# Kernel tuning notes

Measured on AMD Instinct MI355X. Metric: run time of the kernel, lower is better.

The kernel has to match this reference:

```python
import jax, jax.numpy as jnp
import numpy as np

B, S, D, P, H = 32, 1024, 512, 720, 4   # batch, seq_len (=codebook_size), enc_in, pred_len, heads
COMMIT_W, ORTHO_W = 1.0, 0.8


def setup_inputs() -> dict:
    key = jax.random.key(0)
    ks = jax.random.split(key, 6)
    return {
        "x": jax.random.normal(ks[0], (B, S, D), jnp.float32),
        "w_in": jax.random.normal(ks[1], (H * D, D), jnp.float32) * 0.02,   # project_in: dim -> heads*dim
        "b_in": jnp.zeros((H * D,), jnp.float32),
        "embed": jax.random.normal(ks[2], (H, S, D), jnp.float32),          # per-head codebook [h, C, d]
        "w_out": jax.random.normal(ks[3], (D, H * D), jnp.float32) * 0.02,  # project_out: heads*dim -> dim
        "b_out": jnp.zeros((D,), jnp.float32),
        "w_lin": jax.random.normal(ks[4], (P, S), jnp.float32) * 0.02,      # Linear over time axis
        "b_lin": jnp.zeros((P,), jnp.float32),
    }


def reference(x, w_in, b_in, embed, w_out, b_out, w_lin, b_lin):
    C = embed.shape[1]
    # Normalization: subtract last timestep (detached)
    seq_last = jax.lax.stop_gradient(x[:, -1:, :])          # [B,1,D]
    x0 = x - seq_last                                       # [B,S,D]

    # --- VectorQuantize ---
    xi = x0 @ w_in.T + b_in                                 # [B,S,H*D] project_in
    # 'b n (h d) -> h (b n) d' (separate codebook per head)
    f = xi.reshape(B, S, H, D).transpose(2, 0, 1, 3).reshape(H, B * S, D)
    # squared-euclidean distances to codes: [H, B*S, C]
    d2 = (jnp.sum(f * f, -1, keepdims=True)
          - 2.0 * jnp.einsum('hnd,hcd->hnc', f, embed)
          + jnp.sum(embed * embed, -1)[:, None, :])
    ind = jnp.argmin(d2, axis=-1)                           # [H, B*S]
    q = jnp.take_along_axis(embed, ind[:, :, None], axis=1)  # gather -> [H, B*S, D]

    # commitment loss (learnable codebook => quantize NOT detached)
    commit_loss = jnp.mean((q - f) ** 2)
    # orthogonal regularization on full codebook
    normed = embed / jnp.linalg.norm(embed, axis=-1, keepdims=True)
    cs = jnp.einsum('hid,hjd->hij', normed, normed)         # [H,C,C]
    ortho_loss = jnp.sum(cs ** 2) / (H * C * C) - 1.0 / C
    loss = COMMIT_W * commit_loss + ORTHO_W * ortho_loss

    # straight-through estimator
    q_st = f + jax.lax.stop_gradient(q - f)
    # 'h (b n) d -> b n (h d)'
    qo = q_st.reshape(H, B, S, D).transpose(1, 2, 0, 3).reshape(B, S, H * D)
    quantized = qo @ w_out.T + b_out                        # [B,S,D] project_out

    # Linear over the time axis: permute(0,2,1) -> Linear(S->P) -> permute back
    y = jnp.einsum('bnd,pn->bpd', quantized, w_lin) + b_lin[None, :, None]
    y = y + seq_last                                        # [B,P,D]

    indices = ind.reshape(H, B, S).transpose(1, 2, 0)       # [B,S,H]
    return y, indices, loss
```

## Files before the change

kernel.cpp:

```cpp
#include <hip/hip_runtime.h>
#include <stdint.h>

typedef unsigned int u32;
typedef unsigned long long u64;
typedef _Float16 f16;
typedef __attribute__((ext_vector_type(8))) _Float16 f16x8;
typedef __attribute__((ext_vector_type(4))) _Float16 f16x4;
typedef __attribute__((ext_vector_type(2))) _Float16 f16x2;
typedef __attribute__((ext_vector_type(4))) float f32x4;

#define MFMA16(a, b, c) __builtin_amdgcn_mfma_f32_16x16x32_f16((a), (b), (c), 0, 0, 0)
#define MARGIN 2.0f

__device__ __forceinline__ u32 ford(float x) { u32 u = __float_as_uint(x); return (u & 0x80000000u) ? ~u : (u | 0x80000000u); }
__device__ __forceinline__ float iford(u32 v) { u32 u = (v & 0x80000000u) ? (v & 0x7FFFFFFFu) : ~v; return __uint_as_float(u); }
__device__ __forceinline__ int xswz(int i, int n) { return (i & 7) * (n >> 3) + (i >> 3); }

typedef __attribute__((address_space(1))) const unsigned char ga_t;
typedef __attribute__((address_space(3))) unsigned char la_t;
__device__ __forceinline__ void gl16(const void* g, void* l) {
  __builtin_amdgcn_global_load_lds((ga_t*)g, (la_t*)l, 16, 0, 0);
}

template <int LDK>
__device__ __forceinline__ void stg8k(const f16* gRowBase, int ktile, char* sdst, int tid) {
#pragma unroll
  for (int it = 0; it < 2; ++it) {
    const int u = (tid + (it << 8)) << 4;
    const int r = u >> 6, s = (u >> 4) & 3;
    const char* src = (const char*)gRowBase + (size_t)r * (LDK * 2) + ((size_t)ktile << 6) +
                      (size_t)((s ^ ((r >> 1) & 3)) << 4);
    gl16(src, sdst + u);
  }
}

template <int MODE>
__global__ __launch_bounds__(256, (MODE == 0) ? 2 : 3) void gemm2(
    const f16* __restrict__ Ah, const f16* __restrict__ Al,
    const f16* __restrict__ Bh, const f16* __restrict__ Bl,
    int chrows, int ktiles,
    void* __restrict__ out0, void* __restrict__ out1,
    const float* __restrict__ bias, const float* __restrict__ aux,
    u64* __restrict__ slots) {
  constexpr bool K1 = (MODE == 0);
  constexpr int LDK = (MODE == 2 || MODE == 4) ? 1024 : 512;
  constexpr int OPS = K1 ? 4 : 2;
  constexpr int LDS_SZ = (MODE == 3) ? 41472 : (OPS * 16384);
  __shared__ char lds[LDS_SZ];

  const int tid = threadIdx.x;
  const int lane = tid & 63, wid = tid >> 6;
  const int wm = wid >> 1, wn = wid & 1;

  int blkm, blkn, z = 0;
  {
    const int s = xswz(blockIdx.x, gridDim.x);
    if constexpr (MODE == 0) { blkn = s & 15; blkm = s >> 4; }
    else if constexpr (MODE == 1) { blkn = s & 3; blkm = s >> 2; z = blkm >> 3; }
    else if constexpr (MODE == 2) { blkn = s & 3; blkm = (s >> 2) & 3; z = s >> 4; }
    else if constexpr (MODE == 3) { blkn = s & 31; blkm = s >> 5; }
    else { const int r2 = s % 24; blkm = r2 % 6; blkn = r2 / 6; z = s / 24; }
  }

  if constexpr (MODE == 3) {
    u64* candL = (u64*)(lds + 32768);
    int* cntL = (int*)(lds + 40960);
    for (int i = tid; i < 1024; i += 256) candL[i] = ~0ull;
    if (tid < 128) cntL[tid] = 0;
  }

  const f16 *Ab, *Bb, *Alb = nullptr, *Blb = nullptr;
  if constexpr (MODE == 0) {
    Ab = Ah + (size_t)blkm * 65536;
    Alb = Al + (size_t)blkm * 65536;
    Bb = Bh + (size_t)blkn * 65536;
    Blb = Bl + (size_t)blkn * 65536;
  } else if constexpr (MODE == 1) {
    Ab = Ah + (size_t)blkm * 65536;
    Bb = Bh + (size_t)z * 262144 + (size_t)blkn * 65536;
  } else if constexpr (MODE == 2) {
    Ab = Ah + (size_t)z * 524288 + (size_t)blkm * 131072;
    Bb = Bh + (size_t)z * 524288 + (size_t)blkn * 131072;
  } else if constexpr (MODE == 3) {
    const int h = blkn >> 3;
    Ab = Ah + ((size_t)h * chrows + (size_t)blkm * 128) * 512;
    Bb = Bh + (size_t)h * 524288 + (size_t)(blkn & 7) * 65536;
  } else {
    Ab = Ah + (size_t)blkm * 131072;
    Bb = Bh + (size_t)z * 524288 + (size_t)blkn * 131072;
  }

  f32x4 acc[4][4];
#pragma unroll
  for (int i = 0; i < 4; ++i)
#pragma unroll
    for (int j = 0; j < 4; ++j) acc[i][j] = f32x4{0.f, 0.f, 0.f, 0.f};

  constexpr int BUF = OPS * 8192;

  stg8k<LDK>(Ab, 0, lds, tid);
  if constexpr (K1) stg8k<LDK>(Alb, 0, lds + 8192, tid);
  stg8k<LDK>(Bb, 0, lds + (K1 ? 16384 : 8192), tid);
  if constexpr (K1) stg8k<LDK>(Blb, 0, lds + 24576, tid);
  asm volatile("s_waitcnt vmcnt(0)" ::: "memory");
  __syncthreads();

  int cur = 0;
  for (int kc = 0; kc < ktiles; ++kc) {
    if (kc + 1 < ktiles) {
      char* nb = lds + (cur ^ 1) * BUF;
      stg8k<LDK>(Ab, kc + 1, nb, tid);
      if constexpr (K1) stg8k<LDK>(Alb, kc + 1, nb + 8192, tid);
      stg8k<LDK>(Bb, kc + 1, nb + (K1 ? 16384 : 8192), tid);
      if constexpr (K1) stg8k<LDK>(Blb, kc + 1, nb + 24576, tid);
    }
    const char* cb = lds + cur * BUF;
    const int sA = 0, sAl = 8192, sB = K1 ? 16384 : 8192, sBl = 24576;
    f16x8 ah[4], al[4];
#pragma unroll
    for (int mt = 0; mt < 4; ++mt) {
      const int rr = wm * 64 + mt * 16 + (lane & 15);
      const int o = rr * 64 + (((lane >> 4) ^ ((rr >> 1) & 3)) << 4);
      ah[mt] = *(const f16x8*)(cb + sA + o);
      if constexpr (K1) al[mt] = *(const f16x8*)(cb + sAl + o);
    }
#pragma unroll
    for (int nt = 0; nt < 4; ++nt) {
      const int rn = wn * 64 + nt * 16 + (lane & 15);
      const int o = rn * 64 + (((lane >> 4) ^ ((rn >> 1) & 3)) << 4);
      const f16x8 bh = *(const f16x8*)(cb + sB + o);
      f16x8 bl;
      if constexpr (K1) bl = *(const f16x8*)(cb + sBl + o);
#pragma unroll
      for (int mt = 0; mt < 4; ++mt) {
        if constexpr (K1) {
          acc[mt][nt] = MFMA16(al[mt], bh, acc[mt][nt]);
          acc[mt][nt] = MFMA16(ah[mt], bl, acc[mt][nt]);
        }
        acc[mt][nt] = MFMA16(ah[mt], bh, acc[mt][nt]);
      }
    }
    asm volatile("s_waitcnt vmcnt(0)" ::: "memory");
    __syncthreads();
    cur ^= 1;
  }

  if constexpr (MODE == 0) {
    f16* fh = (f16*)out0;
    f16* fl = (f16*)out1;
#pragma unroll
    for (int nt = 0; nt < 4; ++nt) {
      const int gc = blkn * 128 + wn * 64 + nt * 16 + (lane & 15);
      const float bv = bias[gc];
      const int h = gc >> 9, d = gc & 511;
#pragma unroll
      for (int mt = 0; mt < 4; ++mt)
#pragma unroll
        for (int r = 0; r < 4; ++r) {
          const int grow = blkm * 128 + wm * 64 + mt * 16 + ((lane >> 4) << 2) + r;
          const float v = acc[mt][nt][r] * 6.103515625e-05f + bv;
          const f16 hv = (f16)v;
          const size_t off = ((size_t)h * chrows + grow) * 512 + d;
          fh[off] = hv;
          fl[off] = (f16)(v - (float)hv);
        }
    }
  } else if constexpr (MODE == 1) {
    f16* o = (f16*)out0;
#pragma unroll
    for (int nt = 0; nt < 4; ++nt) {
      const int gc = blkn * 128 + wn * 64 + nt * 16 + (lane & 15);
#pragma unroll
      for (int mt = 0; mt < 4; ++mt)
#pragma unroll
        for (int r = 0; r < 4; ++r) {
          const size_t grow = (size_t)blkm * 128 + wm * 64 + mt * 16 + ((lane >> 4) << 2) + r;
          o[grow * 512 + gc] = (f16)acc[mt][nt][r];
        }
    }
  } else if constexpr (MODE == 2) {
    float ssum = 0.f;
#pragma unroll
    for (int mt = 0; mt < 4; ++mt)
#pragma unroll
      for (int nt = 0; nt < 4; ++nt)
#pragma unroll
        for (int r = 0; r < 4; ++r) ssum += acc[mt][nt][r] * acc[mt][nt][r];
#pragma unroll
    for (int o = 1; o < 64; o <<= 1) ssum += __shfl_xor(ssum, o);
    float* wp = (float*)lds;
    if (lane == 0) wp[wid] = ssum;
    __syncthreads();
    if (tid == 0) {
      const float p = wp[0] + wp[1] + wp[2] + wp[3];
      atomicAdd(slots + (blockIdx.x & 63), (u64)llrintf(p * 16777216.f));
    }
  } else if constexpr (MODE == 3) {
    u64* candL = (u64*)(lds + 32768);
    int* cntL = (int*)(lds + 40960);
    u64* candG = (u64*)out0;
    const int h = blkn >> 3;
    float escol[4];
    int cc[4];
#pragma unroll
    for (int nt = 0; nt < 4; ++nt) {
      const int gc = blkn * 128 + wn * 64 + nt * 16 + (lane & 15);
      escol[nt] = aux[gc];
      cc[nt] = gc & 1023;
    }
#pragma unroll
    for (int mt = 0; mt < 4; ++mt)
#pragma unroll
      for (int r = 0; r < 4; ++r) {
        const int row_l = wm * 64 + mt * 16 + ((lane >> 4) << 2) + r;
        float vals[4];
        u64 pk[4];
        u64 mn = ~0ull;
#pragma unroll
        for (int nt = 0; nt < 4; ++nt) {
          const float v = escol[nt] - 2.0f * acc[mt][nt][r];
          vals[nt] = v;
          const u64 p = ((u64)ford(v) << 32) | (u32)cc[nt];
          pk[nt] = p;
          if (p < mn) mn = p;
        }
#pragma unroll
        for (int o = 1; o < 16; o <<= 1) {
          const u64 t = __shfl_xor(mn, o);
          if (t < mn) mn = t;
        }
        const float lim = iford((u32)(mn >> 32)) + MARGIN;
#pragma unroll
        for (int nt = 0; nt < 4; ++nt)
          if (vals[nt] <= lim) {
            const int p = atomicAdd(&cntL[row_l], 1);
            if (p < 8) candL[(row_l << 3) + p] = pk[nt];
          }
      }
    __syncthreads();
#pragma unroll
    for (int j = 0; j < 4; ++j) {
      const int idx = tid * 4 + j;
      const int row_l = idx >> 3, slot = idx & 7;
      const size_t grow = (size_t)blkm * 128 + row_l;
      candG[((size_t)h * chrows + grow) * 64 + (size_t)(blkn & 7) * 8 + slot] = candL[idx];
    }
  } else {
    float* oy = (float*)out0 + (size_t)z * 368640;
    const float* xseq = aux + (size_t)z * 524288 + 523776;
    float sl[4];
    int gd[4];
#pragma unroll
    for (int nt = 0; nt < 4; ++nt) {
      gd[nt] = blkn * 128 + wn * 64 + nt * 16 + (lane & 15);
      sl[nt] = xseq[gd[nt]];
    }
#pragma unroll
    for (int mt = 0; mt < 4; ++mt)
#pragma unroll
      for (int r = 0; r < 4; ++r) {
        const int p = blkm * 128 + wm * 64 + mt * 16 + ((lane >> 4) << 2) + r;
        if (p < 720) {
          const float bp = bias[p];
#pragma unroll
          for (int nt = 0; nt < 4; ++nt) oy[(size_t)p * 512 + gd[nt]] = acc[mt][nt][r] + bp + sl[nt];
        }
      }
  }
}

__global__ __launch_bounds__(256, 4) void rescore_k(
    const u64* __restrict__ candG, const f16* __restrict__ fh,
    const f16* __restrict__ fl, const float* __restrict__ embed,
    int n0, int shCH,
    int* __restrict__ indw, float* __restrict__ indout, u64* __restrict__ cslots) {
  const int tid = threadIdx.x, lane = tid & 63, wid = tid >> 6;
  const int r = blockIdx.x * 4 + wid;
  const int h = r >> shCH, row = r & ((1 << shCH) - 1);
  u64 cu = candG[(size_t)r * 64 + lane];
  u64 mn = cu;
#pragma unroll
  for (int o = 1; o < 64; o <<= 1) { const u64 t = __shfl_xor(mn, o); if (t < mn) mn = t; }
  const float lim = iford((u32)(mn >> 32)) + MARGIN;
  const bool pass = iford((u32)(cu >> 32)) <= lim;
  u64 mask = __ballot(pass);
  float fv[8];
  {
    const size_t fo = (size_t)r * 512 + lane * 8;
    const f16x8 hv = *(const f16x8*)(fh + fo);
    const f16x8 lv = *(const f16x8*)(fl + fo);
#pragma unroll
    for (int j = 0; j < 8; ++j) fv[j] = (float)hv[j] + (float)lv[j];
  }
  double bestd = 1e300;
  int bestc = 0x7FFFFFFF;
  while (mask) {
    const int src = __ffsll((unsigned long long)mask) - 1;
    mask &= mask - 1;
    const int c = (int)(u32)__shfl(cu, src);
    const float* e = embed + ((size_t)h * 1024 + c) * 512 + lane * 8;
    const float4 e0 = *(const float4*)e, e1 = *(const float4*)(e + 4);
    const float ev[8] = {e0.x, e0.y, e0.z, e0.w, e1.x, e1.y, e1.z, e1.w};
    double sd = 0.0;
#pragma unroll
    for (int j = 0; j < 8; ++j) { const double d = (double)fv[j] - (double)ev[j]; sd += d * d; }
#pragma unroll
    for (int o = 1; o < 64; o <<= 1) sd += __shfl_xor(sd, o);
    if (sd < bestd || (sd == bestd && c < bestc)) { bestd = sd; bestc = c; }
  }
  if (lane == 0) {
    const int n = n0 + row;
    indw[(size_t)n * 4 + h] = bestc;
    indout[(size_t)n * 4 + h] = (float)bestc;
    atomicAdd(cslots + (blockIdx.x & 255), (u64)llrint(bestd * 65536.0));
  }
}

__global__ __launch_bounds__(256) void quantize_qT(
    const int* __restrict__ indw, const f16* __restrict__ Ep,
    const float* __restrict__ b_out, f16* __restrict__ qT) {
  const int tid = threadIdx.x;
  const int b = blockIdx.x >> 4, s0 = (blockIdx.x & 15) << 6;
  __shared__ int inds[64][4];
  inds[tid >> 2][tid & 3] = indw[(size_t)(b * 1024 + s0 + (tid >> 2)) * 4 + (tid & 3)];
  __syncthreads();
  const int d0 = tid * 2;
  const float ba0 = b_out[d0], ba1 = b_out[d0 + 1];
  u32 r0[32], r1[32];
  f16 t0 = (f16)0.f, t1 = (f16)0.f;
#pragma unroll
  for (int ss = 0; ss < 64; ++ss) {
    float a0 = ba0, a1 = ba1;
#pragma unroll
    for (int h = 0; h < 4; ++h) {
      const int c = inds[ss][h];
      const f16x2 p = *(const f16x2*)(Ep + (((size_t)h * 1024 + c) * 512 + d0));
      a0 += (float)p[0];
      a1 += (float)p[1];
    }
    const f16 q0 = (f16)a0, q1 = (f16)a1;
    if (ss & 1) {
      f16x2 w0; w0[0] = t0; w0[1] = q0; __builtin_memcpy(&r0[ss >> 1], &w0, 4);
      f16x2 w1; w1[0] = t1; w1[1] = q1; __builtin_memcpy(&r1[ss >> 1], &w1, 4);
    } else { t0 = q0; t1 = q1; }
  }
  const size_t o0 = ((size_t)b * 512 + d0) * 1024 + s0;
#pragma unroll
  for (int i = 0; i < 8; ++i) {
    uint4 v; v.x = r0[4 * i]; v.y = r0[4 * i + 1]; v.z = r0[4 * i + 2]; v.w = r0[4 * i + 3];
    *(uint4*)(qT + o0 + (size_t)i * 8) = v;
  }
  const size_t o1 = o0 + 1024;
#pragma unroll
  for (int i = 0; i < 8; ++i) {
    uint4 v; v.x = r1[4 * i]; v.y = r1[4 * i + 1]; v.z = r1[4 * i + 2]; v.w = r1[4 * i + 3];
    *(uint4*)(qT + o1 + (size_t)i * 8) = v;
  }
}

__global__ __launch_bounds__(256) void prep_x0(const float* __restrict__ x, int n0,
                                               f16* __restrict__ ht, f16* __restrict__ lt) {
  const int id = blockIdx.x * 256 + threadIdx.x;
  const int k8 = id & 63, r = id >> 6;
  const int n = n0 + r, b = n >> 10;
  const float* ap = x + (size_t)n * 512 + k8 * 8;
  const float* sp = x + (size_t)b * 524288 + 523776 + k8 * 8;
  const float4 a0 = *(const float4*)ap, a1 = *(const float4*)(ap + 4);
  const float4 s0 = *(const float4*)sp, s1 = *(const float4*)(sp + 4);
  const float v[8] = {(a0.x - s0.x) * 16.f, (a0.y - s0.y) * 16.f, (a0.z - s0.z) * 16.f,
                      (a0.w - s0.w) * 16.f, (a1.x - s1.x) * 16.f, (a1.y - s1.y) * 16.f,
                      (a1.z - s1.z) * 16.f, (a1.w - s1.w) * 16.f};
  f16x8 hv, lv;
#pragma unroll
  for (int j = 0; j < 8; ++j) { const f16 h = (f16)v[j]; hv[j] = h; lv[j] = (f16)(v[j] - (float)h); }
  const size_t off = (size_t)r * 512 + k8 * 8;
  *(f16x8*)(ht + off) = hv;
  *(f16x8*)(lt + off) = lv;
}

__global__ __launch_bounds__(256) void prep_win(const float* __restrict__ src,
                                                f16* __restrict__ hi, f16* __restrict__ lo) {
  const size_t e = ((size_t)blockIdx.x * 256 + threadIdx.x) * 4;
  const float4 v = *(const float4*)(src + e);
  const float w[4] = {v.x * 1024.f, v.y * 1024.f, v.z * 1024.f, v.w * 1024.f};
  f16x4 hv, lv;
#pragma unroll
  for (int j = 0; j < 4; ++j) { const f16 h = (f16)w[j]; hv[j] = h; lv[j] = (f16)(w[j] - (float)h); }
  *(f16x4*)(hi + e) = hv;
  *(f16x4*)(lo + e) = lv;
}

__global__ __launch_bounds__(256) void prep_embed_k(const float* __restrict__ em,
                                                    f16* __restrict__ ef,
                                                    float* __restrict__ esq,
                                                    float* __restrict__ invn) {
  const int tid = threadIdx.x, lane = tid & 63, wid = tid >> 6;
  const int row = blockIdx.x * 4 + wid;
  const float* er = em + (size_t)row * 512 + lane * 8;
  const float4 a = *(const float4*)er, b = *(const float4*)(er + 4);
  f16x8 v;
  v[0] = (f16)a.x; v[1] = (f16)a.y; v[2] = (f16)a.z; v[3] = (f16)a.w;
  v[4] = (f16)b.x; v[5] = (f16)b.y; v[6] = (f16)b.z; v[7] = (f16)b.w;
  *(f16x8*)(ef + (size_t)row * 512 + lane * 8) = v;
  float s = a.x * a.x + a.y * a.y + a.z * a.z + a.w * a.w +
            b.x * b.x + b.y * b.y + b.z * b.z + b.w * b.w;
#pragma unroll
  for (int o = 1; o < 64; o <<= 1) s += __shfl_xor(s, o);
  if (lane == 0) { esq[row] = s; invn[row] = 1.0f / sqrtf(s); }
}

__global__ __launch_bounds__(256) void prep_wout(const float* __restrict__ src,
                                                 f16* __restrict__ dst) {
  const int id = blockIdx.x * 256 + threadIdx.x;
  const int k8 = id & 63, rg = id >> 6;
  const int d = rg & 511, h = rg >> 9;
  const float* ap = src + (size_t)d * 2048 + h * 512 + k8 * 8;
  const float4 a0 = *(const float4*)ap, a1 = *(const float4*)(ap + 4);
  f16x8 v;
  v[0] = (f16)a0.x; v[1] = (f16)a0.y; v[2] = (f16)a0.z; v[3] = (f16)a0.w;
  v[4] = (f16)a1.x; v[5] = (f16)a1.y; v[6] = (f16)a1.z; v[7] = (f16)a1.w;
  *(f16x8*)(dst + (size_t)h * 262144 + (size_t)d * 512 + k8 * 8) = v;
}

__global__ __launch_bounds__(256) void prep_wlin(const float* __restrict__ src,
                                                 f16* __restrict__ dst) {
  const int id = blockIdx.x * 256 + threadIdx.x;
  const int k8 = id & 127, row = id >> 7;
  float4 a0 = {0.f, 0.f, 0.f, 0.f}, a1 = a0;
  if (row < 720) {
    const float* ap = src + (size_t)row * 1024 + k8 * 8;
    a0 = *(const float4*)ap;
    a1 = *(const float4*)(ap + 4);
  }
  f16x8 v;
  v[0] = (f16)a0.x; v[1] = (f16)a0.y; v[2] = (f16)a0.z; v[3] = (f16)a0.w;
  v[4] = (f16)a1.x; v[5] = (f16)a1.y; v[6] = (f16)a1.z; v[7] = (f16)a1.w;
  *(f16x8*)(dst + (size_t)row * 1024 + k8 * 8) = v;
}

__global__ __launch_bounds__(256) void prep_normT(const float* __restrict__ em,
                                                  const float* __restrict__ invn,
                                                  f16* __restrict__ nT) {
  __shared__ float t[64 * 65];
  const int tid = threadIdx.x;
  const int bx = blockIdx.x;
  const int h = bx >> 7, rem = bx & 127, cb = rem >> 3, db = rem & 7;
  const int c0 = cb * 64, d0 = db * 64;
  const int j = tid & 63, i0 = tid >> 6;
#pragma unroll
  for (int p = 0; p < 16; ++p) {
    const int i = p * 4 + i0;
    t[i * 65 + j] = em[(size_t)h * 524288 + (size_t)(c0 + i) * 512 + d0 + j] * invn[h * 1024 + c0 + i];
  }
  __syncthreads();
#pragma unroll
  for (int p = 0; p < 16; ++p) {
    const int i = p * 4 + i0;
    nT[(size_t)h * 524288 + (size_t)(d0 + i) * 1024 + c0 + j] = (f16)t[j * 65 + i];
  }
}

__global__ void finalize_k(const u64* __restrict__ cs, const u64* __restrict__ gs,
                           float* __restrict__ out) {
  const int lane = threadIdx.x;
  u64 c = cs[lane] + cs[lane + 64] + cs[lane + 128] + cs[lane + 192];
  u64 g = gs[lane];
#pragma unroll
  for (int o = 1; o < 64; o <<= 1) {
    c += __shfl_xor(c, o);
    g += __shfl_xor(g, o);
  }
  if (lane == 0) {
    const double commit = (double)c / 65536.0 / 67108864.0;
    const double ortho = (double)g / 16777216.0 / 4194304.0 - (1.0 / 1024.0);
    out[11927552] = (float)(commit + 0.8 * ortho);
  }
}

__global__ void ws_fail_k(float* out) {
  if (threadIdx.x == 0) out[11927552] = -777777.0f;
}

extern "C" void kernel_launch(void* const* d_in, const int* in_sizes, int n_in,
                              void* d_out, int out_size, void* d_ws, size_t ws_size,
                              hipStream_t stream) {
  (void)in_sizes; (void)n_in; (void)out_size;
  const float* x = (const float*)d_in[0];
  const float* w_in = (const float*)d_in[1];
  const float* b_in = (const float*)d_in[2];
  const float* embed = (const float*)d_in[3];
  const float* w_out = (const float*)d_in[4];
  const float* b_out = (const float*)d_in[5];
  const float* w_lin = (const float*)d_in[6];
  const float* b_lin = (const float*)d_in[7];
  float* out = (float*)d_out;
  char* ws = (char*)d_ws;

  constexpr size_t SZ_WIN = 2097152, SZ_EFT = 4194304, SZ_WOUT = 2097152;
  constexpr size_t SZ_EP = 4194304, SZ_WLIN = 1572864, SZ_NT = 4194304;
  constexpr size_t SZ_SMALL = 16384 + 16384 + 524288 + 2048 + 512;
  constexpr size_t FIXED = SZ_WIN * 2 + SZ_EFT + SZ_WOUT + SZ_EP + SZ_WLIN + SZ_NT + SZ_SMALL;

  int CH = 16384, shCH = 14;
  if (ws_size < FIXED + (size_t)CH * 12288 || (size_t)CH * 6144 < 33554432) {}
  if (ws_size < FIXED + (size_t)16384 * 12288) { CH = 8192; shCH = 13; }
  if (ws_size < FIXED + (size_t)CH * 12288) {
    ws_fail_k<<<1, 64, 0, stream>>>(out);
    return;
  }

  size_t off = 0;
  f16* x0h = (f16*)(ws + off); off += (size_t)CH * 1024;
  f16* x0l = (f16*)(ws + off); off += (size_t)CH * 1024;
  f16* fh = (f16*)(ws + off); off += (size_t)CH * 4096;
  f16* fl = (f16*)(ws + off); off += (size_t)CH * 4096;
  u64* cand = (u64*)(ws + off); off += (size_t)CH * 2048;
  f16* winh = (f16*)(ws + off); off += SZ_WIN;
  f16* winl = (f16*)(ws + off); off += SZ_WIN;
  f16* eft = (f16*)(ws + off); off += SZ_EFT;
  f16* wout = (f16*)(ws + off); off += SZ_WOUT;
  f16* Ep = (f16*)(ws + off); off += SZ_EP;
  f16* wlint = (f16*)(ws + off); off += SZ_WLIN;
  f16* nT = (f16*)(ws + off); off += SZ_NT;
  float* esq = (float*)(ws + off); off += 16384;
  float* invn = (float*)(ws + off); off += 16384;
  int* indw = (int*)(ws + off); off += 524288;
  u64* cslots = (u64*)(ws + off); off += 2048;
  u64* gslots = (u64*)(ws + off); off += 512;
  f16* qT = (f16*)ws;

  hipMemsetAsync((void*)cslots, 0, 2560, stream);

  prep_win<<<1024, 256, 0, stream>>>(w_in, winh, winl);
  prep_embed_k<<<1024, 256, 0, stream>>>(embed, eft, esq, invn);
  prep_normT<<<512, 256, 0, stream>>>(embed, invn, nT);
  prep_wout<<<512, 256, 0, stream>>>(w_out, wout);
  prep_wlin<<<384, 256, 0, stream>>>(w_lin, wlint);

  gemm2<1><<<128, 256, 0, stream>>>(eft, nullptr, wout, nullptr, 0, 16,
                                    Ep, nullptr, nullptr, nullptr, nullptr);
  gemm2<2><<<64, 256, 0, stream>>>(nT, nullptr, nT, nullptr, 0, 32,
                                   nullptr, nullptr, nullptr, nullptr, gslots);

  for (int c0 = 0; c0 < 32768; c0 += CH) {
    prep_x0<<<CH / 4, 256, 0, stream>>>(x, c0, x0h, x0l);
    gemm2<0><<<(CH / 128) * 16, 256, 0, stream>>>(x0h, x0l, winh, winl, CH, 16,
                                                  fh, fl, b_in, nullptr, nullptr);
    gemm2<3><<<(CH / 128) * 32, 256, 0, stream>>>(fh, nullptr, eft, nullptr, CH, 16,
                                                  cand, nullptr, nullptr, esq, nullptr);
    rescore_k<<<CH, 256, 0, stream>>>(cand, fh, fl, embed, c0, shCH,
                                      indw, out + 11796480, cslots);
  }

  quantize_qT<<<512, 256, 0, stream>>>(indw, Ep, b_out, qT);
  gemm2<4><<<768, 256, 0, stream>>>(wlint, nullptr, qT, nullptr, 0, 32,
                                    out, nullptr, b_lin, x, nullptr);
  finalize_k<<<1, 64, 0, stream>>>(cslots, gslots, out);
}
```

Before: 751.8 us.

## Triple-buffer gemm K-loop with partial vmcnt waits and priority boosts

Replaces the double-buffered global-to-LDS pipeline with a compile-time depth-D ring buffer (3 stages for non-split modes) and a fully unrolled K loop. It waits with partial vmcnt counts so later tiles' loads stay in flight, and raises wave priority around the MFMA block. It also reorders MODE 3 block mapping to head-major with per-head codebook tiles and simplifies the candidate min-reduction to float fminf. The extra LDS stage may lower occupancy, and the MODE 3 launch bound drops to 2 waves per SIMD.

```diff
diff --git a/kernel.cpp b/kernel.cpp
--- a/kernel.cpp
+++ b/kernel.cpp
@@ -11,6 +11,7 @@
 
 #define MFMA16(a, b, c) __builtin_amdgcn_mfma_f32_16x16x32_f16((a), (b), (c), 0, 0, 0)
 #define MARGIN 2.0f
+#define WAITV(n) asm volatile("s_waitcnt vmcnt(" #n ")" ::: "memory")
 
 __device__ __forceinline__ u32 ford(float x) { u32 u = __float_as_uint(x); return (u & 0x80000000u) ? ~u : (u | 0x80000000u); }
 __device__ __forceinline__ float iford(u32 v) { u32 u = (v & 0x80000000u) ? (v & 0x7FFFFFFFu) : ~v; return __uint_as_float(u); }
@@ -35,17 +36,20 @@
 }
 
 template <int MODE>
-__global__ __launch_bounds__(256, (MODE == 0) ? 2 : 3) void gemm2(
+__global__ __launch_bounds__(256, (MODE == 0 || MODE == 3) ? 2 : 3) void gemm2(
     const f16* __restrict__ Ah, const f16* __restrict__ Al,
     const f16* __restrict__ Bh, const f16* __restrict__ Bl,
-    int chrows, int ktiles,
+    int chrows,
     void* __restrict__ out0, void* __restrict__ out1,
     const float* __restrict__ bias, const float* __restrict__ aux,
     u64* __restrict__ slots) {
   constexpr bool K1 = (MODE == 0);
   constexpr int LDK = (MODE == 2 || MODE == 4) ? 1024 : 512;
   constexpr int OPS = K1 ? 4 : 2;
-  constexpr int LDS_SZ = (MODE == 3) ? 41472 : (OPS * 16384);
+  constexpr int D = K1 ? 2 : 3;
+  constexpr int KT = (MODE == 2 || MODE == 4) ? 32 : 16;
+  constexpr int BUF = OPS * 8192;
+  constexpr int LDS_SZ = D * BUF + ((MODE == 3) ? 8704 : 0);
   __shared__ char lds[LDS_SZ];
 
   const int tid = threadIdx.x;
@@ -58,13 +62,17 @@
     if constexpr (MODE == 0) { blkn = s & 15; blkm = s >> 4; }
     else if constexpr (MODE == 1) { blkn = s & 3; blkm = s >> 2; z = blkm >> 3; }
     else if constexpr (MODE == 2) { blkn = s & 3; blkm = (s >> 2) & 3; z = s >> 4; }
-    else if constexpr (MODE == 3) { blkn = s & 31; blkm = s >> 5; }
-    else { const int r2 = s % 24; blkm = r2 % 6; blkn = r2 / 6; z = s / 24; }
+    else if constexpr (MODE == 3) {
+      const int bph = (chrows >> 7) << 3;
+      z = s / bph;
+      const int rem = s - z * bph;
+      blkm = rem >> 3; blkn = rem & 7;
+    } else { const int r2 = s % 24; blkm = r2 % 6; blkn = r2 / 6; z = s / 24; }
   }
 
   if constexpr (MODE == 3) {
-    u64* candL = (u64*)(lds + 32768);
-    int* cntL = (int*)(lds + 40960);
+    u64* candL = (u64*)(lds + D * BUF);
+    int* cntL = (int*)(lds + D * BUF + 8192);
     for (int i = tid; i < 1024; i += 256) candL[i] = ~0ull;
     if (tid < 128) cntL[tid] = 0;
   }
@@ -82,9 +90,8 @@
     Ab = Ah + (size_t)z * 524288 + (size_t)blkm * 131072;
     Bb = Bh + (size_t)z * 524288 + (size_t)blkn * 131072;
   } else if constexpr (MODE == 3) {
-    const int h = blkn >> 3;
-    Ab = Ah + ((size_t)h * chrows + (size_t)blkm * 128) * 512;
-    Bb = Bh + (size_t)h * 524288 + (size_t)(blkn & 7) * 65536;
+    Ab = Ah + ((size_t)z * chrows + (size_t)blkm * 128) * 512;
+    Bb = Bh + (size_t)z * 524288 + (size_t)blkn * 65536;
   } else {
     Ab = Ah + (size_t)blkm * 131072;
     Bb = Bh + (size_t)z * 524288 + (size_t)blkn * 131072;
@@ -96,41 +103,46 @@
 #pragma unroll
     for (int j = 0; j < 4; ++j) acc[i][j] = f32x4{0.f, 0.f, 0.f, 0.f};
 
-  constexpr int BUF = OPS * 8192;
-
-  stg8k<LDK>(Ab, 0, lds, tid);
-  if constexpr (K1) stg8k<LDK>(Alb, 0, lds + 8192, tid);
-  stg8k<LDK>(Bb, 0, lds + (K1 ? 16384 : 8192), tid);
-  if constexpr (K1) stg8k<LDK>(Blb, 0, lds + 24576, tid);
-  asm volatile("s_waitcnt vmcnt(0)" ::: "memory");
-  __syncthreads();
-
-  int cur = 0;
-  for (int kc = 0; kc < ktiles; ++kc) {
-    if (kc + 1 < ktiles) {
-      char* nb = lds + (cur ^ 1) * BUF;
-      stg8k<LDK>(Ab, kc + 1, nb, tid);
-      if constexpr (K1) stg8k<LDK>(Alb, kc + 1, nb + 8192, tid);
-      stg8k<LDK>(Bb, kc + 1, nb + (K1 ? 16384 : 8192), tid);
-      if constexpr (K1) stg8k<LDK>(Blb, kc + 1, nb + 24576, tid);
-    }
-    const char* cb = lds + cur * BUF;
-    const int sA = 0, sAl = 8192, sB = K1 ? 16384 : 8192, sBl = 24576;
+#pragma unroll
+  for (int d = 0; d < D - 1; ++d) {
+    char* nb = lds + d * BUF;
+    stg8k<LDK>(Ab, d, nb, tid);
+    if constexpr (K1) stg8k<LDK>(Alb, d, nb + 8192, tid);
+    stg8k<LDK>(Bb, d, nb + (K1 ? 16384 : 8192), tid);
+    if constexpr (K1) stg8k<LDK>(Blb, d, nb + 24576, tid);
+  }
+
+#pragma unroll
+  for (int kc = 0; kc < KT; ++kc) {
+    if (kc + D - 1 < KT) {
+      char* nb = lds + ((kc + D - 1) % D) * BUF;
+      stg8k<LDK>(Ab, kc + D - 1, nb, tid);
+      if constexpr (K1) stg8k<LDK>(Alb, kc + D - 1, nb + 8192, tid);
+      stg8k<LDK>(Bb, kc + D - 1, nb + (K1 ? 16384 : 8192), tid);
+      if constexpr (K1) stg8k<LDK>(Blb, kc + D - 1, nb + 24576, tid);
+    }
+    const int nf = KT - 1 - kc;
+    if (nf >= D - 1) WAITV(8);
+    else if (D == 3 && nf == 1) WAITV(4);
+    else WAITV(0);
+    __builtin_amdgcn_s_barrier();
+    const char* cbuf = lds + (kc % D) * BUF;
     f16x8 ah[4], al[4];
 #pragma unroll
     for (int mt = 0; mt < 4; ++mt) {
       const int rr = wm * 64 + mt * 16 + (lane & 15);
       const int o = rr * 64 + (((lane >> 4) ^ ((rr >> 1) & 3)) << 4);
-      ah[mt] = *(const f16x8*)(cb + sA + o);
-      if constexpr (K1) al[mt] = *(const f16x8*)(cb + sAl + o);
-    }
+      ah[mt] = *(const f16x8*)(cbuf + o);
+      if constexpr (K1) al[mt] = *(const f16x8*)(cbuf + 8192 + o);
+    }
+    __builtin_amdgcn_s_setprio(1);
 #pragma unroll
     for (int nt = 0; nt < 4; ++nt) {
       const int rn = wn * 64 + nt * 16 + (lane & 15);
       const int o = rn * 64 + (((lane >> 4) ^ ((rn >> 1) & 3)) << 4);
-      const f16x8 bh = *(const f16x8*)(cb + sB + o);
+      const f16x8 bh = *(const f16x8*)(cbuf + (K1 ? 16384 : 8192) + o);
       f16x8 bl;
-      if constexpr (K1) bl = *(const f16x8*)(cb + sBl + o);
+      if constexpr (K1) bl = *(const f16x8*)(cbuf + 24576 + o);
 #pragma unroll
       for (int mt = 0; mt < 4; ++mt) {
         if constexpr (K1) {
@@ -140,9 +152,8 @@
         acc[mt][nt] = MFMA16(ah[mt], bh, acc[mt][nt]);
       }
     }
-    asm volatile("s_waitcnt vmcnt(0)" ::: "memory");
-    __syncthreads();
-    cur ^= 1;
+    __builtin_amdgcn_s_setprio(0);
+    __builtin_amdgcn_s_barrier();
   }
 
   if constexpr (MODE == 0) {
@@ -189,6 +200,7 @@
 #pragma unroll
     for (int o = 1; o < 64; o <<= 1) ssum += __shfl_xor(ssum, o);
     float* wp = (float*)lds;
+    __syncthreads();
     if (lane == 0) wp[wid] = ssum;
     __syncthreads();
     if (tid == 0) {
@@ -196,17 +208,16 @@
       atomicAdd(slots + (blockIdx.x & 63), (u64)llrintf(p * 16777216.f));
     }
   } else if constexpr (MODE == 3) {
-    u64* candL = (u64*)(lds + 32768);
-    int* cntL = (int*)(lds + 40960);
+    u64* candL = (u64*)(lds + D * BUF);
+    int* cntL = (int*)(lds + D * BUF + 8192);
     u64* candG = (u64*)out0;
-    const int h = blkn >> 3;
+    const int h = z;
     float escol[4];
     int cc[4];
 #pragma unroll
     for (int nt = 0; nt < 4; ++nt) {
-      const int gc = blkn * 128 + wn * 64 + nt * 16 + (lane & 15);
-      escol[nt] = aux[gc];
-      cc[nt] = gc & 1023;
+      cc[nt] = blkn * 128 + wn * 64 + nt * 16 + (lane & 15);
+      escol[nt] = aux[h * 1024 + cc[nt]];
     }
 #pragma unroll
     for (int mt = 0; mt < 4; ++mt)
@@ -214,27 +225,21 @@
       for (int r = 0; r < 4; ++r) {
         const int row_l = wm * 64 + mt * 16 + ((lane >> 4) << 2) + r;
         float vals[4];
-        u64 pk[4];
-        u64 mn = ~0ull;
+        float mn = 3.4e38f;
 #pragma unroll
         for (int nt = 0; nt < 4; ++nt) {
           const float v = escol[nt] - 2.0f * acc[mt][nt][r];
           vals[nt] = v;
-          const u64 p = ((u64)ford(v) << 32) | (u32)cc[nt];
-          pk[nt] = p;
-          if (p < mn) mn = p;
+          mn = fminf(mn, v);
         }
 #pragma unroll
-        for (int o = 1; o < 16; o <<= 1) {
-          const u64 t = __shfl_xor(mn, o);
-          if (t < mn) mn = t;
-        }
-        const float lim = iford((u32)(mn >> 32)) + MARGIN;
+        for (int o = 1; o < 16; o <<= 1) mn = fminf(mn, __shfl_xor(mn, o));
+        const float lim = mn + MARGIN;
 #pragma unroll
         for (int nt = 0; nt < 4; ++nt)
           if (vals[nt] <= lim) {
             const int p = atomicAdd(&cntL[row_l], 1);
-            if (p < 8) candL[(row_l << 3) + p] = pk[nt];
+            if (p < 8) candL[(row_l << 3) + p] = ((u64)ford(vals[nt]) << 32) | (u32)cc[nt];
           }
       }
     __syncthreads();
@@ -243,7 +248,7 @@
       const int idx = tid * 4 + j;
       const int row_l = idx >> 3, slot = idx & 7;
       const size_t grow = (size_t)blkm * 128 + row_l;
-      candG[((size_t)h * chrows + grow) * 64 + (size_t)(blkn & 7) * 8 + slot] = candL[idx];
+      candG[((size_t)h * chrows + grow) * 64 + (size_t)blkn * 8 + slot] = candL[idx];
     }
   } else {
     float* oy = (float*)out0 + (size_t)z * 368640;
@@ -502,7 +507,6 @@
   constexpr size_t FIXED = SZ_WIN * 2 + SZ_EFT + SZ_WOUT + SZ_EP + SZ_WLIN + SZ_NT + SZ_SMALL;
 
   int CH = 16384, shCH = 14;
-  if (ws_size < FIXED + (size_t)CH * 12288 || (size_t)CH * 6144 < 33554432) {}
   if (ws_size < FIXED + (size_t)16384 * 12288) { CH = 8192; shCH = 13; }
   if (ws_size < FIXED + (size_t)CH * 12288) {
     ws_fail_k<<<1, 64, 0, stream>>>(out);
@@ -537,23 +541,23 @@
   prep_wout<<<512, 256, 0, stream>>>(w_out, wout);
   prep_wlin<<<384, 256, 0, stream>>>(w_lin, wlint);
 
-  gemm2<1><<<128, 256, 0, stream>>>(eft, nullptr, wout, nullptr, 0, 16,
+  gemm2<1><<<128, 256, 0, stream>>>(eft, nullptr, wout, nullptr, 0,
                                     Ep, nullptr, nullptr, nullptr, nullptr);
-  gemm2<2><<<64, 256, 0, stream>>>(nT, nullptr, nT, nullptr, 0, 32,
+  gemm2<2><<<64, 256, 0, stream>>>(nT, nullptr, nT, nullptr, 0,
                                    nullptr, nullptr, nullptr, nullptr, gslots);
 
   for (int c0 = 0; c0 < 32768; c0 += CH) {
     prep_x0<<<CH / 4, 256, 0, stream>>>(x, c0, x0h, x0l);
-    gemm2<0><<<(CH / 128) * 16, 256, 0, stream>>>(x0h, x0l, winh, winl, CH, 16,
+    gemm2<0><<<(CH / 128) * 16, 256, 0, stream>>>(x0h, x0l, winh, winl, CH,
                                                   fh, fl, b_in, nullptr, nullptr);
-    gemm2<3><<<(CH / 128) * 32, 256, 0, stream>>>(fh, nullptr, eft, nullptr, CH, 16,
+    gemm2<3><<<(CH / 128) * 32, 256, 0, stream>>>(fh, nullptr, eft, nullptr, CH,
                                                   cand, nullptr, nullptr, esq, nullptr);
     rescore_k<<<CH, 256, 0, stream>>>(cand, fh, fl, embed, c0, shCH,
                                       indw, out + 11796480, cslots);
   }
 
   quantize_qT<<<512, 256, 0, stream>>>(indw, Ep, b_out, qT);
-  gemm2<4><<<768, 256, 0, stream>>>(wlint, nullptr, qT, nullptr, 0, 32,
+  gemm2<4><<<768, 256, 0, stream>>>(wlint, nullptr, qT, nullptr, 0,
                                     out, nullptr, b_lin, x, nullptr);
   finalize_k<<<1, 64, 0, stream>>>(cslots, gslots, out);
 }
```

Result: faster. 708.3 us (-5.8%).
